# Performance work log

Hardware: AMD Instinct MI355X
Metric: run time of the kernel (lower is better)

The kernel has to match this reference:

```python
import jax, jax.numpy as jnp
import numpy as np

B, S, HIDDEN = 4, 2048, 1024
NUM_EXPERTS = 8
TOP_K = 4
EPS = 1e-6


def setup_inputs() -> dict:
    key = jax.random.key(0)
    k0, k1, k2 = jax.random.split(key, 3)
    x = jax.random.normal(k0, (B, S, HIDDEN), dtype=jnp.float32)
    Wg = jax.random.normal(k1, (HIDDEN, NUM_EXPERTS), dtype=jnp.float32) * 0.02
    bg = jnp.zeros((NUM_EXPERTS,), dtype=jnp.float32)
    W = jax.random.normal(k2, (NUM_EXPERTS, HIDDEN, HIDDEN), dtype=jnp.float32) * 0.02
    b = jnp.zeros((NUM_EXPERTS, HIDDEN), dtype=jnp.float32)
    return {"x": x, "Wg": Wg, "bg": bg, "W": W, "b": b}


def reference(x, Wg, bg, W, b):
    Bb, Ss, D = x.shape
    xf = x.reshape(-1, D)                       # [T, D]
    T = xf.shape[0]

    # --- router ---
    router_logits = xf @ Wg + bg                # [T, E]
    router_probs = jax.nn.softmax(router_logits, axis=-1)
    top_k_probs, top_k_indices = jax.lax.top_k(router_probs, TOP_K)  # [T, K]
    top_k_weights = top_k_probs / (top_k_probs.sum(axis=-1, keepdims=True) + EPS)
    expert_mask = jax.nn.one_hot(top_k_indices, NUM_EXPERTS, dtype=jnp.float32).sum(axis=1)  # [T, E]

    # --- experts: original computes every expert on every token then masks;
    # same math expressed as one batched GEMM + gather ---
    all_out = jnp.einsum('td,edf->etf', xf, W) + b[:, None, :]  # [E, T, D]
    sel = all_out[top_k_indices.T, jnp.arange(T)[None, :]]      # [K, T, D]
    moe_output = jnp.einsum('tk,ktd->td', top_k_weights, sel).reshape(Bb, Ss, D)

    # --- load-balancing aux loss ---
    aux_loss = jnp.dot(expert_mask.mean(axis=0), router_probs.mean(axis=0)) * NUM_EXPERTS
    return moe_output, aux_loss
```

## Files before the change

### kernel.cpp

```cpp
#include <hip/hip_runtime.h>
#include <hip/hip_bf16.h>

#define T_TOK 8192
#define DH    1024
#define NE    8
#define TK    4

typedef unsigned short u16;
typedef __bf16 bf16x8 __attribute__((ext_vector_type(8)));
typedef float  f32x4  __attribute__((ext_vector_type(4)));

__device__ __forceinline__ u16 f2b(float f) {
    union { float f; unsigned u; } v; v.f = f;
    unsigned u = v.u;
    u += 0x7FFFu + ((u >> 16) & 1u);
    return (u16)(u >> 16);
}
__device__ __forceinline__ float b2f(u16 h) {
    union { unsigned u; float f; } v; v.u = ((unsigned)h) << 16;
    return v.f;
}
__device__ __forceinline__ void glds16(const u16* g, u16* l) {
    __builtin_amdgcn_global_load_lds((const __attribute__((address_space(1))) void*)g,
                                     (__attribute__((address_space(3))) void*)l, 16, 0, 0);
}

#define FENCE() asm volatile("" ::: "memory")
#define SBAR()  do { FENCE(); __builtin_amdgcn_s_barrier(); FENCE(); } while (0)
#define WAITLGKM0() do { asm volatile("s_waitcnt lgkmcnt(0)" ::: "memory"); \
                         __builtin_amdgcn_sched_barrier(0); } while (0)
#define WAITVM(n) asm volatile("s_waitcnt vmcnt(" #n ")" ::: "memory")

__global__ __launch_bounds__(512) void prep_kernel(
    const float* __restrict__ W, u16* __restrict__ wbt,
    const float* __restrict__ x, const float* __restrict__ Wg, const float* __restrict__ bg,
    u16* __restrict__ xb,
    int* __restrict__ bucket_tok, float* __restrict__ bucket_w,
    int* __restrict__ tk_e, float* __restrict__ tk_w,
    int* __restrict__ cnt, float* __restrict__ probsum)
{
    __shared__ float tile2[2][64][65];
    __shared__ int   lcnt[NE];
    __shared__ float lprob[NE];
    __shared__ int   gbase[NE];

    const int bid = blockIdx.x;
    const int tid = threadIdx.x;

    if (bid < 1024) {
        const int half = tid >> 8;
        const int tloc = tid & 255;
        const int r  = tloc >> 4;
        const int c4 = (tloc & 15) * 4;
        float (*tile)[65] = tile2[half];
        const int jc = bid * 2 + half;
        const int f0 = (jc & 15) * 64;
        const int d0 = ((jc >> 4) & 15) * 64;
        const int e  = jc >> 8;
        const float* src = W + ((size_t)e << 20) + (size_t)d0 * DH + f0;
        #pragma unroll
        for (int i = 0; i < 4; i++) {
            const int row = i * 16 + r;
            const float4 v = *(const float4*)(src + (size_t)row * DH + c4);
            tile[row][c4]     = v.x;
            tile[row][c4 + 1] = v.y;
            tile[row][c4 + 2] = v.z;
            tile[row][c4 + 3] = v.w;
        }
        __syncthreads();
        u16* dst = wbt + ((size_t)e << 20) + (size_t)f0 * DH + d0;
        #pragma unroll
        for (int i = 0; i < 4; i++) {
            const int orow = i * 16 + r;
            ushort4 o;
            o.x = f2b(tile[c4][orow]);
            o.y = f2b(tile[c4 + 1][orow]);
            o.z = f2b(tile[c4 + 2][orow]);
            o.w = f2b(tile[c4 + 3][orow]);
            *(ushort4*)(dst + (size_t)orow * DH + c4) = o;
        }
        return;
    }

    const int wv = tid >> 6, lane = tid & 63;
    const int t = (bid - 1024) * 8 + wv;
    if (tid < NE) { lcnt[tid] = 0; lprob[tid] = 0.f; }
    __syncthreads();

    float a[NE] = {};
    {
        const float* xr = x + (size_t)t * DH;
        u16* xbr = xb + (size_t)t * DH;
        const float4* wg = (const float4*)Wg;
        #pragma unroll
        for (int it = 0; it < 4; it++) {
            const int d = it * 256 + lane * 4;
            const float4 v = *(const float4*)(xr + d);
            ushort4 o;
            o.x = f2b(v.x); o.y = f2b(v.y); o.z = f2b(v.z); o.w = f2b(v.w);
            *(ushort4*)(xbr + d) = o;
            const float4 w0l = wg[2 * (d + 0)], w0h = wg[2 * (d + 0) + 1];
            const float4 w1l = wg[2 * (d + 1)], w1h = wg[2 * (d + 1) + 1];
            const float4 w2l = wg[2 * (d + 2)], w2h = wg[2 * (d + 2) + 1];
            const float4 w3l = wg[2 * (d + 3)], w3h = wg[2 * (d + 3) + 1];
            a[0] += v.x * w0l.x + v.y * w1l.x + v.z * w2l.x + v.w * w3l.x;
            a[1] += v.x * w0l.y + v.y * w1l.y + v.z * w2l.y + v.w * w3l.y;
            a[2] += v.x * w0l.z + v.y * w1l.z + v.z * w2l.z + v.w * w3l.z;
            a[3] += v.x * w0l.w + v.y * w1l.w + v.z * w2l.w + v.w * w3l.w;
            a[4] += v.x * w0h.x + v.y * w1h.x + v.z * w2h.x + v.w * w3h.x;
            a[5] += v.x * w0h.y + v.y * w1h.y + v.z * w2h.y + v.w * w3h.y;
            a[6] += v.x * w0h.z + v.y * w1h.z + v.z * w2h.z + v.w * w3h.z;
            a[7] += v.x * w0h.w + v.y * w1h.w + v.z * w2h.w + v.w * w3h.w;
        }
    }
    #pragma unroll
    for (int e = 0; e < NE; e++) {
        float v = a[e];
        #pragma unroll
        for (int off = 32; off > 0; off >>= 1) v += __shfl_down(v, off);
        a[e] = v;
    }

    int idx4[TK]; float w4[TK]; int off4[TK];
    if (lane == 0) {
        float logits[NE], probs[NE];
        float mx = -1e30f;
        #pragma unroll
        for (int e = 0; e < NE; e++) { logits[e] = a[e] + bg[e]; mx = fmaxf(mx, logits[e]); }
        float Z = 0.f;
        #pragma unroll
        for (int e = 0; e < NE; e++) { probs[e] = expf(logits[e] - mx); Z += probs[e]; }
        const float rZ = 1.f / Z;
        #pragma unroll
        for (int e = 0; e < NE; e++) probs[e] *= rZ;

        float rem2[NE];
        #pragma unroll
        for (int e = 0; e < NE; e++) rem2[e] = probs[e];
        float s4 = 0.f;
        #pragma unroll
        for (int k = 0; k < TK; k++) {
            int best = 0; float bv = rem2[0];
            #pragma unroll
            for (int e = 1; e < NE; e++) if (rem2[e] > bv) { bv = rem2[e]; best = e; }
            idx4[k] = best; w4[k] = bv; s4 += bv; rem2[best] = -1e30f;
        }
        const float rs = 1.f / (s4 + 1e-6f);
        #pragma unroll
        for (int k = 0; k < TK; k++) {
            w4[k] *= rs;
            tk_e[t * TK + k] = idx4[k];
            tk_w[t * TK + k] = w4[k];
            off4[k] = atomicAdd(&lcnt[idx4[k]], 1);
        }
        #pragma unroll
        for (int e = 0; e < NE; e++) atomicAdd(&lprob[e], probs[e]);
    }
    __syncthreads();
    if (tid < NE) {
        gbase[tid] = atomicAdd(&cnt[tid], lcnt[tid]);
        atomicAdd(&probsum[tid], lprob[tid]);
    }
    __syncthreads();
    if (lane == 0) {
        #pragma unroll
        for (int k = 0; k < TK; k++) {
            const int e = idx4[k];
            const int slot = gbase[e] + off4[k];
            bucket_tok[e * T_TOK + slot] = (t << 2) | k;
            bucket_w[e * T_TOK + slot]   = w4[k];
        }
    }
}

__global__ __launch_bounds__(512, 2) void moe_gemm_kernel(
    const u16* __restrict__ xb, const u16* __restrict__ wbt,
    const int* __restrict__ bucket_tok, const float* __restrict__ bucket_w,
    const int* __restrict__ cnt, u16* __restrict__ y)
{
    __shared__ u16 As[2][256 * 64];
    __shared__ u16 Bs[2][256 * 64];
    __shared__ int   s_tok[256];
    __shared__ float s_w[256];

    const int tid  = threadIdx.x;
    const int lane = tid & 63;
    const int wid  = tid >> 6;
    const int wr   = wid >> 2;
    const int wc   = wid & 3;
    const int fr   = lane & 15;
    const int fq   = (lane >> 4) * 8;
    const int swz  = (fr & 7) << 3;
    const int gsw  = ((lane & 7) ^ (lane >> 3)) * 8;
    const int crow = lane >> 3;

    const int ALb = 2 * wid + (wid >= 4 ? 8 : 0);
    const int AHb = ALb + 8;
    const int BLb = (wid >> 1) * 8 + (wid & 1) * 2;
    const int BHb = BLb + 4;

    const int e = blockIdx.x & 7;
    const int c = blockIdx.x >> 3;
    const int M = cnt[e];

    for (int j = 0; j < 4; ++j) {
        const int idx = j * 32 + c;
        const int mb = idx >> 2;
        const int nb = idx & 3;
        const int m0 = mb << 8;
        if (m0 >= M) continue;
        const int n0 = nb << 8;

        __syncthreads();
        if (tid < 256) {
            const int slot = m0 + tid;
            if (slot < M) {
                s_tok[tid] = bucket_tok[e * T_TOK + slot];
                s_w[tid]   = bucket_w[e * T_TOK + slot];
            } else { s_tok[tid] = -1; s_w[tid] = 0.f; }
        }
        __syncthreads();

        const int rAL0 = ALb * 8 + crow, rAL1 = rAL0 + 8;
        const int rAH0 = AHb * 8 + crow, rAH1 = rAH0 + 8;
        const int tAL0 = s_tok[rAL0], tAL1 = s_tok[rAL1];
        const int tAH0 = s_tok[rAH0], tAH1 = s_tok[rAH1];
        const u16* gAL0 = xb + (size_t)(tAL0 >= 0 ? (tAL0 >> 2) : 0) * DH + gsw;
        const u16* gAL1 = xb + (size_t)(tAL1 >= 0 ? (tAL1 >> 2) : 0) * DH + gsw;
        const u16* gAH0 = xb + (size_t)(tAH0 >= 0 ? (tAH0 >> 2) : 0) * DH + gsw;
        const u16* gAH1 = xb + (size_t)(tAH1 >= 0 ? (tAH1 >> 2) : 0) * DH + gsw;
        const u16* wbe  = wbt + ((size_t)e << 20);
        const u16* gBL0 = wbe + (size_t)(n0 + BLb * 8 + crow) * DH + gsw;
        const u16* gBL1 = gBL0 + (size_t)8 * DH;
        const u16* gBH0 = wbe + (size_t)(n0 + BHb * 8 + crow) * DH + gsw;
        const u16* gBH1 = gBH0 + (size_t)8 * DH;

        f32x4 acc[8][4] = {};

        #pragma unroll
        for (int kt = 0; kt < 2; kt++) {
            const int ko = kt * 64; const int p = kt;
            glds16(gAL0 + ko, &As[p][ALb * 512]); glds16(gAL1 + ko, &As[p][(ALb + 1) * 512]);
            glds16(gAH0 + ko, &As[p][AHb * 512]); glds16(gAH1 + ko, &As[p][(AHb + 1) * 512]);
            glds16(gBL0 + ko, &Bs[p][BLb * 512]); glds16(gBL1 + ko, &Bs[p][(BLb + 1) * 512]);
            glds16(gBH0 + ko, &Bs[p][BHb * 512]); glds16(gBH1 + ko, &Bs[p][(BHb + 1) * 512]);
        }
        WAITVM(8);
        SBAR();

        const int arow = (wr * 128 + fr) * 64;
        const int brow = (wc * 64  + fr) * 64;
        const int c0 = fq ^ swz;
        const int c1 = (32 + fq) ^ swz;

        bf16x8 afL[4][2], afH[4][2], bfL[2][2], bfH[2][2];

        for (int kt = 0; kt < 16; ++kt) {
            const int p = kt & 1;
            const u16* Ap = &As[p][0];
            const u16* Bp = &Bs[p][0];

            #pragma unroll
            for (int mi = 0; mi < 4; mi++) {
                afL[mi][0] = *(const bf16x8*)&Ap[arow + mi * 1024 + c0];
                afL[mi][1] = *(const bf16x8*)&Ap[arow + mi * 1024 + c1];
            }
            #pragma unroll
            for (int nj = 0; nj < 2; nj++) {
                bfL[nj][0] = *(const bf16x8*)&Bp[brow + nj * 1024 + c0];
                bfL[nj][1] = *(const bf16x8*)&Bp[brow + nj * 1024 + c1];
            }
            if (kt >= 1 && kt <= 14) {
                const int ko = (kt + 1) * 64; const int q = (kt + 1) & 1;
                glds16(gAH0 + ko, &As[q][AHb * 512]);
                glds16(gAH1 + ko, &As[q][(AHb + 1) * 512]);
            }
            asm volatile("s_waitcnt lgkmcnt(8)" ::: "memory");
            SBAR(); WAITLGKM0();
            __builtin_amdgcn_s_setprio(1);
            #pragma unroll
            for (int mi = 0; mi < 4; mi++)
                #pragma unroll
                for (int nj = 0; nj < 2; nj++) {
                    acc[mi][nj] = __builtin_amdgcn_mfma_f32_16x16x32_bf16(afL[mi][0], bfL[nj][0], acc[mi][nj], 0, 0, 0);
                    acc[mi][nj] = __builtin_amdgcn_mfma_f32_16x16x32_bf16(afL[mi][1], bfL[nj][1], acc[mi][nj], 0, 0, 0);
                }
            __builtin_amdgcn_s_setprio(0);
            SBAR();

            #pragma unroll
            for (int nj = 0; nj < 2; nj++) {
                bfH[nj][0] = *(const bf16x8*)&Bp[brow + (nj + 2) * 1024 + c0];
                bfH[nj][1] = *(const bf16x8*)&Bp[brow + (nj + 2) * 1024 + c1];
            }
            if (kt <= 13) {
                const int ko = (kt + 2) * 64;
                glds16(gAL0 + ko, &As[p][ALb * 512]);
                glds16(gAL1 + ko, &As[p][(ALb + 1) * 512]);
            }
            SBAR(); WAITLGKM0();
            __builtin_amdgcn_s_setprio(1);
            #pragma unroll
            for (int mi = 0; mi < 4; mi++)
                #pragma unroll
                for (int nj = 0; nj < 2; nj++) {
                    acc[mi][nj + 2] = __builtin_amdgcn_mfma_f32_16x16x32_bf16(afL[mi][0], bfH[nj][0], acc[mi][nj + 2], 0, 0, 0);
                    acc[mi][nj + 2] = __builtin_amdgcn_mfma_f32_16x16x32_bf16(afL[mi][1], bfH[nj][1], acc[mi][nj + 2], 0, 0, 0);
                }
            __builtin_amdgcn_s_setprio(0);
            SBAR();

            #pragma unroll
            for (int mi = 0; mi < 4; mi++) {
                afH[mi][0] = *(const bf16x8*)&Ap[arow + (mi + 4) * 1024 + c0];
                afH[mi][1] = *(const bf16x8*)&Ap[arow + (mi + 4) * 1024 + c1];
            }
            if (kt <= 13) {
                const int ko = (kt + 2) * 64;
                glds16(gBL0 + ko, &Bs[p][BLb * 512]);
                glds16(gBL1 + ko, &Bs[p][(BLb + 1) * 512]);
            }
            SBAR(); WAITLGKM0();
            __builtin_amdgcn_s_setprio(1);
            #pragma unroll
            for (int mi = 0; mi < 4; mi++)
                #pragma unroll
                for (int nj = 0; nj < 2; nj++) {
                    acc[mi + 4][nj + 2] = __builtin_amdgcn_mfma_f32_16x16x32_bf16(afH[mi][0], bfH[nj][0], acc[mi + 4][nj + 2], 0, 0, 0);
                    acc[mi + 4][nj + 2] = __builtin_amdgcn_mfma_f32_16x16x32_bf16(afH[mi][1], bfH[nj][1], acc[mi + 4][nj + 2], 0, 0, 0);
                }
            __builtin_amdgcn_s_setprio(0);
            SBAR();

            if (kt <= 13) {
                const int ko = (kt + 2) * 64;
                glds16(gBH0 + ko, &Bs[p][BHb * 512]);
                glds16(gBH1 + ko, &Bs[p][(BHb + 1) * 512]);
            }
            __builtin_amdgcn_s_setprio(1);
            #pragma unroll
            for (int mi = 0; mi < 4; mi++)
                #pragma unroll
                for (int nj = 0; nj < 2; nj++) {
                    acc[mi + 4][nj] = __builtin_amdgcn_mfma_f32_16x16x32_bf16(afH[mi][0], bfL[nj][0], acc[mi + 4][nj], 0, 0, 0);
                    acc[mi + 4][nj] = __builtin_amdgcn_mfma_f32_16x16x32_bf16(afH[mi][1], bfL[nj][1], acc[mi + 4][nj], 0, 0, 0);
                }
            __builtin_amdgcn_s_setprio(0);
            if (kt <= 13)      WAITVM(6);
            else if (kt == 14) WAITVM(0);
            SBAR();
        }

        const int cl = lane & 15;
        const int rb = (lane >> 4) * 4;
        #pragma unroll
        for (int mi = 0; mi < 8; mi++) {
            #pragma unroll
            for (int r = 0; r < 4; r++) {
                const int srow = wr * 128 + mi * 16 + rb + r;
                const int tok = s_tok[srow];
                if (tok < 0) continue;
                const float w = s_w[srow];
                u16* yr = y + (size_t)tok * DH + (n0 + wc * 64 + cl);
                #pragma unroll
                for (int nj = 0; nj < 4; nj++)
                    yr[nj * 16] = f2b(acc[mi][nj][r] * w);
            }
        }
    }
}

__global__ __launch_bounds__(256) void combine_kernel(
    const u16* __restrict__ y, const int* __restrict__ tk_e, const float* __restrict__ tk_w,
    const float* __restrict__ bexp,
    const int* __restrict__ cnt, const float* __restrict__ probsum,
    float* __restrict__ out, float* __restrict__ out_aux)
{
    if (blockIdx.x == 0 && threadIdx.x == 0) {
        float s = 0.f;
        for (int e = 0; e < NE; e++) s += (float)cnt[e] * probsum[e];
        out_aux[0] = s * (float)NE / ((float)T_TOK * (float)T_TOK);
    }
    const int t = blockIdx.x * 2 + (threadIdx.x >> 7);
    const int c = (threadIdx.x & 127) * 8;
    float o[8] = {};
    #pragma unroll
    for (int k = 0; k < TK; k++) {
        const int e   = tk_e[t * TK + k];
        const float w = tk_w[t * TK + k];
        const u16* yp = y + ((size_t)(t * TK + k)) * DH + c;
        const ushort4 y0 = *(const ushort4*)(yp);
        const ushort4 y1 = *(const ushort4*)(yp + 4);
        const float4  b0 = *(const float4*)(bexp + (size_t)e * DH + c);
        const float4  b1 = *(const float4*)(bexp + (size_t)e * DH + c + 4);
        o[0] += b2f(y0.x) + w * b0.x;
        o[1] += b2f(y0.y) + w * b0.y;
        o[2] += b2f(y0.z) + w * b0.z;
        o[3] += b2f(y0.w) + w * b0.w;
        o[4] += b2f(y1.x) + w * b1.x;
        o[5] += b2f(y1.y) + w * b1.y;
        o[6] += b2f(y1.z) + w * b1.z;
        o[7] += b2f(y1.w) + w * b1.w;
    }
    float4 ov0 = {o[0], o[1], o[2], o[3]};
    float4 ov1 = {o[4], o[5], o[6], o[7]};
    *(float4*)(out + (size_t)t * DH + c)     = ov0;
    *(float4*)(out + (size_t)t * DH + c + 4) = ov1;
}

extern "C" void kernel_launch(void* const* d_in, const int* in_sizes, int n_in,
                              void* d_out, int out_size, void* d_ws, size_t ws_size,
                              hipStream_t stream)
{
    const float* x  = (const float*)d_in[0];
    const float* Wg = (const float*)d_in[1];
    const float* bg = (const float*)d_in[2];
    const float* W  = (const float*)d_in[3];
    const float* b  = (const float*)d_in[4];
    float* out = (float*)d_out;

    char* ws = (char*)d_ws;
    u16*   xb         = (u16*)(ws);
    u16*   wbt        = (u16*)(ws + 16777216);
    u16*   y          = (u16*)(ws + 33554432);
    int*   bucket_tok = (int*)(ws + 100663296);
    float* bucket_w   = (float*)(ws + 100925440);
    int*   tk_e       = (int*)(ws + 101187584);
    float* tk_w       = (float*)(ws + 101318656);
    int*   cnt        = (int*)(ws + 101449728);
    float* probsum    = (float*)(ws + 101449760);

    hipMemsetAsync(cnt, 0, 64, stream);

    prep_kernel<<<2048, 512, 0, stream>>>(W, wbt, x, Wg, bg, xb,
                                          bucket_tok, bucket_w, tk_e, tk_w, cnt, probsum);
    moe_gemm_kernel<<<dim3(256), 512, 0, stream>>>(xb, wbt, bucket_tok, bucket_w, cnt, y);
    combine_kernel<<<4096, 256, 0, stream>>>(y, tk_e, tk_w, b, cnt, probsum, out, out + (size_t)T_TOK * DH);
}
```

Measured before the change: 253.4 us.

## Split partial expert tiles into separate 64-row tail GEMM kernel

```diff
diff --git a/kernel.cpp b/kernel.cpp
--- a/kernel.cpp
+++ b/kernel.cpp
@@ -208,16 +208,13 @@
         const int mb = idx >> 2;
         const int nb = idx & 3;
         const int m0 = mb << 8;
-        if (m0 >= M) continue;
+        if (m0 + 256 > M) continue;
         const int n0 = nb << 8;
 
         __syncthreads();
         if (tid < 256) {
-            const int slot = m0 + tid;
-            if (slot < M) {
-                s_tok[tid] = bucket_tok[e * T_TOK + slot];
-                s_w[tid]   = bucket_w[e * T_TOK + slot];
-            } else { s_tok[tid] = -1; s_w[tid] = 0.f; }
+            s_tok[tid] = bucket_tok[e * T_TOK + m0 + tid];
+            s_w[tid]   = bucket_w[e * T_TOK + m0 + tid];
         }
         __syncthreads();
 
@@ -225,10 +222,10 @@
         const int rAH0 = AHb * 8 + crow, rAH1 = rAH0 + 8;
         const int tAL0 = s_tok[rAL0], tAL1 = s_tok[rAL1];
         const int tAH0 = s_tok[rAH0], tAH1 = s_tok[rAH1];
-        const u16* gAL0 = xb + (size_t)(tAL0 >= 0 ? (tAL0 >> 2) : 0) * DH + gsw;
-        const u16* gAL1 = xb + (size_t)(tAL1 >= 0 ? (tAL1 >> 2) : 0) * DH + gsw;
-        const u16* gAH0 = xb + (size_t)(tAH0 >= 0 ? (tAH0 >> 2) : 0) * DH + gsw;
-        const u16* gAH1 = xb + (size_t)(tAH1 >= 0 ? (tAH1 >> 2) : 0) * DH + gsw;
+        const u16* gAL0 = xb + (size_t)(tAL0 >> 2) * DH + gsw;
+        const u16* gAL1 = xb + (size_t)(tAL1 >> 2) * DH + gsw;
+        const u16* gAH0 = xb + (size_t)(tAH0 >> 2) * DH + gsw;
+        const u16* gAH1 = xb + (size_t)(tAH1 >> 2) * DH + gsw;
         const u16* wbe  = wbt + ((size_t)e << 20);
         const u16* gBL0 = wbe + (size_t)(n0 + BLb * 8 + crow) * DH + gsw;
         const u16* gBL1 = gBL0 + (size_t)8 * DH;
@@ -359,13 +356,118 @@
             for (int r = 0; r < 4; r++) {
                 const int srow = wr * 128 + mi * 16 + rb + r;
                 const int tok = s_tok[srow];
-                if (tok < 0) continue;
                 const float w = s_w[srow];
                 u16* yr = y + (size_t)tok * DH + (n0 + wc * 64 + cl);
                 #pragma unroll
                 for (int nj = 0; nj < 4; nj++)
                     yr[nj * 16] = f2b(acc[mi][nj][r] * w);
             }
+        }
+    }
+}
+
+__global__ __launch_bounds__(512) void moe_gemm_tail_kernel(
+    const u16* __restrict__ xb, const u16* __restrict__ wbt,
+    const int* __restrict__ bucket_tok, const float* __restrict__ bucket_w,
+    const int* __restrict__ cnt, u16* __restrict__ y)
+{
+    __shared__ u16 As[2][64 * 64];
+    __shared__ u16 Bs[2][256 * 64];
+    __shared__ int   s_tok[64];
+    __shared__ float s_w[64];
+
+    const int e  = blockIdx.z;
+    const int sb = blockIdx.y;
+    const int nb = blockIdx.x;
+    const int M  = cnt[e];
+    const int m0 = ((M >> 8) << 8) + sb * 64;
+    if (m0 >= M) return;
+    const int n0 = nb << 8;
+
+    const int tid  = threadIdx.x;
+    const int lane = tid & 63;
+    const int w8   = tid >> 6;
+    const int fr   = lane & 15;
+    const int fq   = (lane >> 4) * 8;
+    const int swz  = (fr & 7) << 3;
+    const int gsw  = ((lane & 7) ^ (lane >> 3)) * 8;
+    const int crow = lane >> 3;
+
+    if (tid < 64) {
+        const int slot = m0 + tid;
+        if (slot < M) { s_tok[tid] = bucket_tok[e * T_TOK + slot]; s_w[tid] = bucket_w[e * T_TOK + slot]; }
+        else          { s_tok[tid] = -1;                           s_w[tid] = 0.f; }
+    }
+    __syncthreads();
+
+    const int tA = s_tok[w8 * 8 + crow];
+    const u16* gA = xb + (size_t)(tA >= 0 ? (tA >> 2) : 0) * DH + gsw;
+    const u16* wbe = wbt + ((size_t)e << 20);
+    const u16* gB0 = wbe + (size_t)(n0 + (4 * w8 + 0) * 8 + crow) * DH + gsw;
+    const u16* gB1 = wbe + (size_t)(n0 + (4 * w8 + 1) * 8 + crow) * DH + gsw;
+    const u16* gB2 = wbe + (size_t)(n0 + (4 * w8 + 2) * 8 + crow) * DH + gsw;
+    const u16* gB3 = wbe + (size_t)(n0 + (4 * w8 + 3) * 8 + crow) * DH + gsw;
+
+    f32x4 acc[4][2] = {};
+
+    #define TSTAGE(kt) do { const int p_ = (kt) & 1; const int ko_ = (kt) * 64;         \
+        glds16(gA  + ko_, &As[p_][w8 * 512]);                                           \
+        glds16(gB0 + ko_, &Bs[p_][(4 * w8 + 0) * 512]);                                 \
+        glds16(gB1 + ko_, &Bs[p_][(4 * w8 + 1) * 512]);                                 \
+        glds16(gB2 + ko_, &Bs[p_][(4 * w8 + 2) * 512]);                                 \
+        glds16(gB3 + ko_, &Bs[p_][(4 * w8 + 3) * 512]); } while (0)
+
+    TSTAGE(0); TSTAGE(1);
+    WAITVM(5);
+    SBAR();
+
+    const int c0 = fq ^ swz;
+    const int c1 = (32 + fq) ^ swz;
+
+    for (int kt = 0; kt < 16; ++kt) {
+        const int p = kt & 1;
+        bf16x8 af[4][2], bf[2][2];
+        #pragma unroll
+        for (int mi = 0; mi < 4; mi++) {
+            af[mi][0] = *(const bf16x8*)&As[p][(mi * 16 + fr) * 64 + c0];
+            af[mi][1] = *(const bf16x8*)&As[p][(mi * 16 + fr) * 64 + c1];
+        }
+        #pragma unroll
+        for (int nj = 0; nj < 2; nj++) {
+            bf[nj][0] = *(const bf16x8*)&Bs[p][(w8 * 32 + nj * 16 + fr) * 64 + c0];
+            bf[nj][1] = *(const bf16x8*)&Bs[p][(w8 * 32 + nj * 16 + fr) * 64 + c1];
+        }
+        WAITLGKM0();
+        __builtin_amdgcn_s_setprio(1);
+        #pragma unroll
+        for (int mi = 0; mi < 4; mi++)
+            #pragma unroll
+            for (int nj = 0; nj < 2; nj++) {
+                acc[mi][nj] = __builtin_amdgcn_mfma_f32_16x16x32_bf16(af[mi][0], bf[nj][0], acc[mi][nj], 0, 0, 0);
+                acc[mi][nj] = __builtin_amdgcn_mfma_f32_16x16x32_bf16(af[mi][1], bf[nj][1], acc[mi][nj], 0, 0, 0);
+            }
+        __builtin_amdgcn_s_setprio(0);
+        SBAR();
+        if (kt + 2 < 16) { TSTAGE(kt + 2); WAITVM(5); }
+        else if (kt == 14) WAITVM(0);
+        if (kt < 15) SBAR();
+    }
+    #undef TSTAGE
+
+    const int cl = lane & 15;
+    const int rb = (lane >> 4) * 4;
+    #pragma unroll
+    for (int mi = 0; mi < 4; mi++) {
+        #pragma unroll
+        for (int r = 0; r < 4; r++) {
+            const int srow = mi * 16 + rb + r;
+            const int tok = s_tok[srow];
+            if (tok < 0) continue;
+            const float w = s_w[srow];
+            u16* yr = y + (size_t)tok * DH + (n0 + w8 * 32 + cl);
+            #pragma unroll
+            for (int nj = 0; nj < 2; nj++)
+                yr[nj * 16] = f2b(acc[mi][nj][r] * w);
         }
     }
 }
@@ -435,5 +537,6 @@
     prep_kernel<<<2048, 512, 0, stream>>>(W, wbt, x, Wg, bg, xb,
                                           bucket_tok, bucket_w, tk_e, tk_w, cnt, probsum);
     moe_gemm_kernel<<<dim3(256), 512, 0, stream>>>(xb, wbt, bucket_tok, bucket_w, cnt, y);
+    moe_gemm_tail_kernel<<<dim3(4, 4, NE), 512, 0, stream>>>(xb, wbt, bucket_tok, bucket_w, cnt, y);
     combine_kernel<<<4096, 256, 0, stream>>>(y, tk_e, tk_w, b, cnt, probsum, out, out + (size_t)T_TOK * DH);
 }
```

New measurement: 245.9 us. 1.03x faster.
